# Kernel tuning notes

Measured on AMD Instinct MI355X. Metric: run time of the kernel, lower is better.

## Reference

```python
import jax, jax.numpy as jnp
import numpy as np

N_SRC, N_DST, DEG = 100000, 50000, 16
NODE_IN, EDGE_IN, HID = 128, 64, 64
E = N_DST * DEG


def sparsemax(z):
    # z: [..., K]; sparsemax along last axis (Martins & Astudillo)
    z = z - jnp.max(z, axis=-1, keepdims=True)
    zs = -jnp.sort(-z, axis=-1)  # descending sort
    k_range = jnp.arange(1, z.shape[-1] + 1, dtype=z.dtype)
    cs = jnp.cumsum(zs, axis=-1)
    is_gt = (1.0 + k_range * zs > cs).astype(z.dtype)
    k = jnp.max(is_gt * k_range, axis=-1, keepdims=True)
    tau = (jnp.sum(is_gt * zs, axis=-1, keepdims=True) - 1.0) / k
    return jnp.maximum(z - tau, 0.0)


def setup_inputs() -> dict:
    key = jax.random.key(0)
    ks = jax.random.split(key, 8)
    s = 0.02
    return {
        "node_features": jax.random.normal(ks[0], (N_SRC, NODE_IN), jnp.float32),
        "edge_features": jax.random.normal(ks[1], (E, EDGE_IN), jnp.float32),
        "src_idx": jax.random.randint(ks[2], (E,), 0, N_SRC, jnp.int32),
        "We": s * jax.random.normal(ks[3], (EDGE_IN, HID), jnp.float32),
        "be": jnp.zeros((HID,), jnp.float32),
        "Wa": s * jax.random.normal(ks[4], (EDGE_IN, HID), jnp.float32),
        "ba": jnp.zeros((HID,), jnp.float32),
        "wa": s * jax.random.normal(ks[5], (HID,), jnp.float32),
        "Wo": s * jax.random.normal(ks[6], (NODE_IN + HID, HID), jnp.float32),
        "bo": jnp.zeros((HID,), jnp.float32),
        "Wn": s * jax.random.normal(ks[7], (NODE_IN + HID, HID), jnp.float32),
        "bn": jnp.zeros((HID,), jnp.float32),
        "n_dst": N_DST,
        "deg": DEG,
    }


def reference(node_features, edge_features, src_idx, We, be, Wa, ba, wa, Wo, bo, Wn, bn, n_dst, deg):
    # dropout is identity in eval / p=0
    h_dst = node_features[:n_dst]                               # [n_dst, node_in]
    # message_func: per-edge transforms
    e_out = jax.nn.relu(edge_features @ We + be)                # [E, hid]
    a = jax.nn.leaky_relu((edge_features @ Wa + ba) @ wa)       # [E]
    h_src_e = node_features[src_idx]                            # gather [E, node_in]
    m = jax.nn.relu(jnp.concatenate([h_src_e, e_out], axis=-1) @ Wo + bo)  # [E, hid]
    # reduce_func: mailbox is [n_dst, deg, .] (fixed in-degree graph)
    a = a.reshape(n_dst, deg)
    m = m.reshape(n_dst, deg, -1)
    alpha = sparsemax(a)                                        # [n_dst, deg]
    h_neigh = jnp.einsum('nd,ndh->nh', alpha, m)                # [n_dst, hid]
    # node update
    return jax.nn.relu(jnp.concatenate([h_dst, h_neigh], axis=-1) @ Wn + bn)
```

## Files before the change

kernel.cpp:

```cpp
#include <hip/hip_runtime.h>


#define ND 50000
#define NS 100000

typedef __bf16 bf16x8 __attribute__((ext_vector_type(8)));
typedef float f32x4 __attribute__((ext_vector_type(4)));

__device__ __forceinline__ void sync_wave() {
  asm volatile("s_waitcnt lgkmcnt(0)" ::: "memory");
}

__device__ __forceinline__ unsigned short f2bf(float x) {
  unsigned u = __float_as_uint(x);
  u += 0x7fffu + ((u >> 16) & 1u);
  return (unsigned short)(u >> 16);
}
__device__ __forceinline__ float bf2f(unsigned short u) {
  return __uint_as_float((unsigned)u << 16);
}

union Frag8 { bf16x8 v; unsigned u32[4]; };

__device__ __forceinline__ bf16x8 pack8(const float* fr) {
  Frag8 f;
  #pragma unroll
  for (int j = 0; j < 4; ++j) {
    unsigned lo = __float_as_uint(fr[2 * j]) + 0x8000u;
    unsigned hi = __float_as_uint(fr[2 * j + 1]) + 0x8000u;
    f.u32[j] = __builtin_amdgcn_perm(hi, lo, 0x07060302);
  }
  return f.v;
}

#define MFMA(a, b, c) __builtin_amdgcn_mfma_f32_16x16x32_bf16((a), (b), (c), 0, 0, 0)

extern "C" __global__ void gteast_prep(const float* __restrict__ Wa,
                                       const float* __restrict__ ba,
                                       const float* __restrict__ wa,
                                       float* __restrict__ vc) {
  __shared__ float red[260];
  const int tid = threadIdx.x, k = tid >> 2, p = tid & 3;
  float s = 0.f;
  for (int h = 16 * p; h < 16 * p + 16; ++h) s += Wa[k * 64 + h] * wa[h];
  red[tid] = s;
  if (tid < 4) {
    float sc = 0.f;
    for (int h = 16 * tid; h < 16 * tid + 16; ++h) sc += ba[h] * wa[h];
    red[256 + tid] = sc;
  }
  __syncthreads();
  if (p == 0) vc[k] = red[4 * k] + red[4 * k + 1] + red[4 * k + 2] + red[4 * k + 3];
  if (tid == 0) vc[64] = red[256] + red[257] + red[258] + red[259];
}

extern "C" __global__ void __launch_bounds__(256, 3)
gteast_src(const float* __restrict__ nf, const float* __restrict__ Wo,
           unsigned short* __restrict__ y) {
  __shared__ unsigned short WuT[64 * 136];
  const int tid = threadIdx.x;
  for (int i = tid; i < 128 * 64; i += 256) {
    int k = i >> 6, n = i & 63;
    WuT[n * 136 + k] = f2bf(Wo[i]);
  }
  __syncthreads();

  const int lane = tid & 63, w = tid >> 6, q = lane >> 4, t = lane & 15;
  const int tile = blockIdx.x * 4 + w;
  if (tile >= NS / 16) return;
  const int r0 = tile * 16;

  float raw[8];
  bf16x8 af[4];
  const float* hp = nf + (long)(r0 + t) * 128 + q * 8;
  #pragma unroll
  for (int kc = 0; kc < 4; ++kc) {
    float4 a0 = *reinterpret_cast<const float4*>(hp + kc * 32);
    float4 a1 = *reinterpret_cast<const float4*>(hp + kc * 32 + 4);
    raw[0] = a0.x; raw[1] = a0.y; raw[2] = a0.z; raw[3] = a0.w;
    raw[4] = a1.x; raw[5] = a1.y; raw[6] = a1.z; raw[7] = a1.w;
    af[kc] = pack8(raw);
  }
  #pragma unroll
  for (int nt = 0; nt < 4; ++nt) {
    f32x4 c = {0.f, 0.f, 0.f, 0.f};
    #pragma unroll
    for (int kc = 0; kc < 4; ++kc)
      c = MFMA(af[kc], *reinterpret_cast<const bf16x8*>(&WuT[(nt * 16 + t) * 136 + kc * 32 + q * 8]), c);
    #pragma unroll
    for (int r = 0; r < 4; ++r)
      y[(long)(r0 + 4 * q + r) * 64 + nt * 16 + t] = f2bf(c[r]);
  }
}

extern "C" __global__ void __launch_bounds__(256, 3)
gteast_edge(const float* __restrict__ ef, const int* __restrict__ src_idx,
            const float* __restrict__ We, const float* __restrict__ be,
            const float* __restrict__ Wo, const float* __restrict__ bo,
            const float* __restrict__ vc, const unsigned short* __restrict__ y,
            float* __restrict__ hn_out) {
  __shared__ unsigned short WeT[64 * 72];
  __shared__ unsigned short WoLoT[64 * 72];
  __shared__ unsigned short Elds[4][16 * 72];
  __shared__ float vls[68];

  const int tid = threadIdx.x;
  for (int i = tid; i < 64 * 64; i += 256) {
    int k = i >> 6, n = i & 63;
    WeT[n * 72 + k] = f2bf(We[i]);
  }
  for (int i = tid; i < 64 * 64; i += 256) {
    int k = i >> 6, n = i & 63;
    WoLoT[n * 72 + k] = f2bf(Wo[(128 + k) * 64 + n]);
  }
  if (tid < 65) vls[tid] = vc[tid];
  __syncthreads();

  const int lane = tid & 63, w = tid >> 6;
  const int q = lane >> 4, t = lane & 15;
  const int wid = blockIdx.x * 4 + w;
  if (wid * 8 >= ND) return;

  unsigned short* E = Elds[w];
  const float cval = vls[64];
  float beL[4], boL[4];
  #pragma unroll
  for (int nt = 0; nt < 4; ++nt) { beL[nt] = be[nt * 16 + t]; boL[nt] = bo[nt * 16 + t]; }
  float vsl[16];
  #pragma unroll
  for (int j = 0; j < 8; ++j) { vsl[j] = vls[q * 8 + j]; vsl[8 + j] = vls[32 + q * 8 + j]; }

  const int si0 = src_idx[wid * 128 + lane];
  const int si1 = src_idx[wid * 128 + 64 + lane];

  const long ebase = (long)(wid * 128);

  float4 efn[4];
  {
    const float* er = ef + (ebase + t) * 64 + q * 8;
    efn[0] = *reinterpret_cast<const float4*>(er);
    efn[1] = *reinterpret_cast<const float4*>(er + 4);
    efn[2] = *reinterpret_cast<const float4*>(er + 32);
    efn[3] = *reinterpret_cast<const float4*>(er + 36);
  }
  unsigned short yv[16];
  #pragma unroll
  for (int r = 0; r < 4; ++r) {
    const int s0 = __shfl(si0, 4 * q + r);
    const unsigned short* yp = y + (long)s0 * 64 + t;
    #pragma unroll
    for (int nt = 0; nt < 4; ++nt) yv[r * 4 + nt] = yp[nt * 16];
  }

  for (int it = 0; it < 8; ++it) {
    const int n = wid * 8 + it;
    const int itn = it < 7 ? it + 1 : 7;

    float fe[16];
    fe[0] = efn[0].x; fe[1] = efn[0].y; fe[2] = efn[0].z; fe[3] = efn[0].w;
    fe[4] = efn[1].x; fe[5] = efn[1].y; fe[6] = efn[1].z; fe[7] = efn[1].w;
    fe[8] = efn[2].x; fe[9] = efn[2].y; fe[10] = efn[2].z; fe[11] = efn[2].w;
    fe[12] = efn[3].x; fe[13] = efn[3].y; fe[14] = efn[3].z; fe[15] = efn[3].w;
    {
      const float* er = ef + (ebase + itn * 16 + t) * 64 + q * 8;
      efn[0] = *reinterpret_cast<const float4*>(er);
      efn[1] = *reinterpret_cast<const float4*>(er + 4);
      efn[2] = *reinterpret_cast<const float4*>(er + 32);
      efn[3] = *reinterpret_cast<const float4*>(er + 36);
    }

    float ap = 0.f;
    #pragma unroll
    for (int j = 0; j < 16; ++j) ap += fe[j] * vsl[j];
    ap += __shfl_xor(ap, 16);
    ap += __shfl_xor(ap, 32);
    float a = ap + cval;
    a = a > 0.f ? a : 0.01f * a;

    const bf16x8 e0 = pack8(fe), e1 = pack8(fe + 8);
    #pragma unroll
    for (int nt = 0; nt < 4; ++nt) {
      f32x4 c = {0.f, 0.f, 0.f, 0.f};
      c = MFMA(e0, *reinterpret_cast<const bf16x8*>(&WeT[(nt * 16 + t) * 72 + q * 8]), c);
      c = MFMA(e1, *reinterpret_cast<const bf16x8*>(&WeT[(nt * 16 + t) * 72 + 32 + q * 8]), c);
      #pragma unroll
      for (int r = 0; r < 4; ++r) {
        float vv = fmaxf(c[r] + beL[nt], 0.f);
        E[(4 * q + r) * 72 + nt * 16 + t] = f2bf(vv);
      }
    }
    sync_wave();

    bf16x8 af4 = *reinterpret_cast<const bf16x8*>(&E[t * 72 + q * 8]);
    bf16x8 af5 = *reinterpret_cast<const bf16x8*>(&E[t * 72 + 32 + q * 8]);

    f32x4 accM[4];
    #pragma unroll
    for (int nt = 0; nt < 4; ++nt) {
      f32x4 c = {0.f, 0.f, 0.f, 0.f};
      c = MFMA(af4, *reinterpret_cast<const bf16x8*>(&WoLoT[(nt * 16 + t) * 72 + q * 8]), c);
      c = MFMA(af5, *reinterpret_cast<const bf16x8*>(&WoLoT[(nt * 16 + t) * 72 + 32 + q * 8]), c);
      #pragma unroll
      for (int r = 0; r < 4; ++r)
        c[r] = fmaxf(c[r] + bf2f(yv[r * 4 + nt]) + boL[nt], 0.f);
      accM[nt] = c;
    }
    sync_wave();

    #pragma unroll
    for (int r = 0; r < 4; ++r) {
      const int idx = 16 * itn + 4 * q + r;
      const int sn = (itn < 4) ? __shfl(si0, idx) : __shfl(si1, idx - 64);
      const unsigned short* yp = y + (long)sn * 64 + t;
      #pragma unroll
      for (int nt = 0; nt < 4; ++nt) yv[r * 4 + nt] = yp[nt * 16];
    }

    const float z = a;
    float cp = 0.f, sp = 0.f;
    #pragma unroll
    for (int r = 0; r < 4; ++r) {
      float zj = __shfl(z, 4 * q + r, 16);
      const bool ge = (zj >= z);
      cp += ge ? 1.f : 0.f;
      sp += ge ? zj : 0.f;
    }
    cp += __shfl_xor(cp, 16); sp += __shfl_xor(sp, 16);
    cp += __shfl_xor(cp, 32); sp += __shfl_xor(sp, 32);
    const bool valid = 1.f + cp * z > sp;
    float kf = valid ? cp : 0.f;
    float sv = valid ? sp : 0.f;
    #pragma unroll
    for (int m = 1; m < 16; m <<= 1) {
      float ok = __shfl_xor(kf, m), os = __shfl_xor(sv, m);
      if (ok > kf) { kf = ok; sv = os; }
    }
    const float tau = (sv - 1.f) / kf;
    const float alpha = fmaxf(a - tau, 0.f);

    float al[4];
    #pragma unroll
    for (int r = 0; r < 4; ++r) al[r] = __shfl(alpha, 4 * q + r);
    float p[4];
    #pragma unroll
    for (int nt = 0; nt < 4; ++nt) {
      p[nt] = al[0] * accM[nt][0] + al[1] * accM[nt][1] +
              al[2] * accM[nt][2] + al[3] * accM[nt][3];
      p[nt] += __shfl_xor(p[nt], 16);
      p[nt] += __shfl_xor(p[nt], 32);
    }
    const float pown = (q == 0) ? p[0] : (q == 1) ? p[1] : (q == 2) ? p[2] : p[3];
    hn_out[(long)n * 64 + lane] = pown;
  }
}

extern "C" __global__ void __launch_bounds__(256, 3)
gteast_edge_fb(const float* __restrict__ nf, const float* __restrict__ ef,
               const int* __restrict__ src_idx,
               const float* __restrict__ We, const float* __restrict__ be,
               const float* __restrict__ Wo, const float* __restrict__ bo,
               const float* __restrict__ vc,
               float* __restrict__ hn_out) {
  __shared__ unsigned short WeT[64 * 72];
  __shared__ unsigned short WoT[64 * 200];
  __shared__ unsigned short Elds[4][16 * 72];
  __shared__ float vls[68];

  const int tid = threadIdx.x;
  for (int i = tid; i < 64 * 64; i += 256) {
    int k = i >> 6, n = i & 63;
    WeT[n * 72 + k] = f2bf(We[i]);
  }
  for (int i = tid; i < 192 * 64; i += 256) {
    int k = i >> 6, n = i & 63;
    WoT[n * 200 + k] = f2bf(Wo[i]);
  }
  if (tid < 65) vls[tid] = vc[tid];
  __syncthreads();

  const int lane = tid & 63, w = tid >> 6;
  const int q = lane >> 4, t = lane & 15;
  const int wid = blockIdx.x * 4 + w;
  if (wid * 8 >= ND) return;

  unsigned short* E = Elds[w];
  const float cval = vls[64];
  float beL[4], boL[4];
  #pragma unroll
  for (int nt = 0; nt < 4; ++nt) { beL[nt] = be[nt * 16 + t]; boL[nt] = bo[nt * 16 + t]; }
  float vsl[16];
  #pragma unroll
  for (int j = 0; j < 8; ++j) { vsl[j] = vls[q * 8 + j]; vsl[8 + j] = vls[32 + q * 8 + j]; }

  const int si0 = src_idx[wid * 128 + lane];
  const int si1 = src_idx[wid * 128 + 64 + lane];
  const long ebase = (long)(wid * 128);

  float4 efn[4];
  {
    const float* er = ef + (ebase + t) * 64 + q * 8;
    efn[0] = *reinterpret_cast<const float4*>(er);
    efn[1] = *reinterpret_cast<const float4*>(er + 4);
    efn[2] = *reinterpret_cast<const float4*>(er + 32);
    efn[3] = *reinterpret_cast<const float4*>(er + 36);
  }
  float hraw[32];
  {
    const int s0 = __shfl(si0, t);
    const float* hp = nf + (long)s0 * 128 + q * 8;
    #pragma unroll
    for (int kc = 0; kc < 4; ++kc) {
      float4 a0 = *reinterpret_cast<const float4*>(hp + kc * 32);
      float4 a1 = *reinterpret_cast<const float4*>(hp + kc * 32 + 4);
      hraw[kc * 8 + 0] = a0.x; hraw[kc * 8 + 1] = a0.y; hraw[kc * 8 + 2] = a0.z; hraw[kc * 8 + 3] = a0.w;
      hraw[kc * 8 + 4] = a1.x; hraw[kc * 8 + 5] = a1.y; hraw[kc * 8 + 6] = a1.z; hraw[kc * 8 + 7] = a1.w;
    }
  }

  for (int it = 0; it < 8; ++it) {
    const int n = wid * 8 + it;
    const int itn = it < 7 ? it + 1 : 7;

    float fe[16];
    fe[0] = efn[0].x; fe[1] = efn[0].y; fe[2] = efn[0].z; fe[3] = efn[0].w;
    fe[4] = efn[1].x; fe[5] = efn[1].y; fe[6] = efn[1].z; fe[7] = efn[1].w;
    fe[8] = efn[2].x; fe[9] = efn[2].y; fe[10] = efn[2].z; fe[11] = efn[2].w;
    fe[12] = efn[3].x; fe[13] = efn[3].y; fe[14] = efn[3].z; fe[15] = efn[3].w;
    {
      const float* er = ef + (ebase + itn * 16 + t) * 64 + q * 8;
      efn[0] = *reinterpret_cast<const float4*>(er);
      efn[1] = *reinterpret_cast<const float4*>(er + 4);
      efn[2] = *reinterpret_cast<const float4*>(er + 32);
      efn[3] = *reinterpret_cast<const float4*>(er + 36);
    }

    float ap = 0.f;
    #pragma unroll
    for (int j = 0; j < 16; ++j) ap += fe[j] * vsl[j];
    ap += __shfl_xor(ap, 16);
    ap += __shfl_xor(ap, 32);
    float a = ap + cval;
    a = a > 0.f ? a : 0.01f * a;

    const bf16x8 e0 = pack8(fe), e1 = pack8(fe + 8);
    #pragma unroll
    for (int nt = 0; nt < 4; ++nt) {
      f32x4 c = {0.f, 0.f, 0.f, 0.f};
      c = MFMA(e0, *reinterpret_cast<const bf16x8*>(&WeT[(nt * 16 + t) * 72 + q * 8]), c);
      c = MFMA(e1, *reinterpret_cast<const bf16x8*>(&WeT[(nt * 16 + t) * 72 + 32 + q * 8]), c);
      #pragma unroll
      for (int r = 0; r < 4; ++r) {
        float vv = fmaxf(c[r] + beL[nt], 0.f);
        E[(4 * q + r) * 72 + nt * 16 + t] = f2bf(vv);
      }
    }
    sync_wave();

    bf16x8 af[6];
    #pragma unroll
    for (int kc = 0; kc < 4; ++kc) af[kc] = pack8(hraw + kc * 8);
    af[4] = *reinterpret_cast<const bf16x8*>(&E[t * 72 + q * 8]);
    af[5] = *reinterpret_cast<const bf16x8*>(&E[t * 72 + 32 + q * 8]);

    {
      const int sn = (itn < 4) ? __shfl(si0, 16 * itn + t)
                               : __shfl(si1, 16 * (itn - 4) + t);
      const float* hp = nf + (long)sn * 128 + q * 8;
      #pragma unroll
      for (int kc = 0; kc < 4; ++kc) {
        float4 a0 = *reinterpret_cast<const float4*>(hp + kc * 32);
        float4 a1 = *reinterpret_cast<const float4*>(hp + kc * 32 + 4);
        hraw[kc * 8 + 0] = a0.x; hraw[kc * 8 + 1] = a0.y; hraw[kc * 8 + 2] = a0.z; hraw[kc * 8 + 3] = a0.w;
        hraw[kc * 8 + 4] = a1.x; hraw[kc * 8 + 5] = a1.y; hraw[kc * 8 + 6] = a1.z; hraw[kc * 8 + 7] = a1.w;
      }
    }

    f32x4 accM[4];
    #pragma unroll
    for (int nt = 0; nt < 4; ++nt) {
      f32x4 c = {0.f, 0.f, 0.f, 0.f};
      #pragma unroll
      for (int kc = 0; kc < 6; ++kc)
        c = MFMA(af[kc], *reinterpret_cast<const bf16x8*>(&WoT[(nt * 16 + t) * 200 + kc * 32 + q * 8]), c);
      #pragma unroll
      for (int r = 0; r < 4; ++r) c[r] = fmaxf(c[r] + boL[nt], 0.f);
      accM[nt] = c;
    }
    sync_wave();

    float zz = a;
    #pragma unroll
    for (int k = 2; k <= 16; k <<= 1) {
      #pragma unroll
      for (int j = k >> 1; j > 0; j >>= 1) {
        float o = __shfl_xor(zz, j);
        const bool upper = (t & j) != 0;
        const bool desc = (t & k) == 0;
        zz = (upper != desc) ? fmaxf(zz, o) : fminf(zz, o);
      }
    }
    float cs = zz;
    #pragma unroll
    for (int off = 1; off < 16; off <<= 1) {
      float o = __shfl_up(cs, off, 16);
      cs += (t >= off) ? o : 0.f;
    }
    const bool gt = 1.f + (float)(t + 1) * zz > cs;
    float kf = gt ? (float)(t + 1) : 0.f;
    float sv = gt ? zz : 0.f;
    #pragma unroll
    for (int m = 1; m < 16; m <<= 1) {
      kf = fmaxf(kf, __shfl_xor(kf, m));
      sv += __shfl_xor(sv, m);
    }
    const float tau = (sv - 1.f) / kf;
    const float alpha = fmaxf(a - tau, 0.f);

    float al[4];
    #pragma unroll
    for (int r = 0; r < 4; ++r) al[r] = __shfl(alpha, 4 * q + r);
    float p[4];
    #pragma unroll
    for (int nt = 0; nt < 4; ++nt) {
      p[nt] = al[0] * accM[nt][0] + al[1] * accM[nt][1] +
              al[2] * accM[nt][2] + al[3] * accM[nt][3];
      p[nt] += __shfl_xor(p[nt], 16);
      p[nt] += __shfl_xor(p[nt], 32);
    }
    const float pown = (q == 0) ? p[0] : (q == 1) ? p[1] : (q == 2) ? p[2] : p[3];
    hn_out[(long)n * 64 + lane] = pown;
  }
}

extern "C" __global__ void __launch_bounds__(256, 3)
gteast_out(const float* __restrict__ nf, const float* __restrict__ Wn,
           const float* __restrict__ bn, float* __restrict__ out) {
  __shared__ unsigned short WnT[64 * 200];
  const int tid = threadIdx.x;
  for (int i = tid; i < 192 * 64; i += 256) {
    int k = i >> 6, nn = i & 63;
    WnT[nn * 200 + k] = f2bf(Wn[i]);
  }
  __syncthreads();

  const int lane = tid & 63, w = tid >> 6, q = lane >> 4, t = lane & 15;
  const int tile = blockIdx.x * 4 + w;
  if (tile >= ND / 16) return;
  const int r0 = tile * 16;

  float bnL[4];
  #pragma unroll
  for (int nt = 0; nt < 4; ++nt) bnL[nt] = bn[nt * 16 + t];

  float raw[8];
  bf16x8 af[6];
  const float* hp = nf + (long)(r0 + t) * 128 + q * 8;
  #pragma unroll
  for (int kc = 0; kc < 4; ++kc) {
    float4 a0 = *reinterpret_cast<const float4*>(hp + kc * 32);
    float4 a1 = *reinterpret_cast<const float4*>(hp + kc * 32 + 4);
    raw[0] = a0.x; raw[1] = a0.y; raw[2] = a0.z; raw[3] = a0.w;
    raw[4] = a1.x; raw[5] = a1.y; raw[6] = a1.z; raw[7] = a1.w;
    af[kc] = pack8(raw);
  }
  const float* gp = out + (long)(r0 + t) * 64 + q * 8;
  #pragma unroll
  for (int kc = 0; kc < 2; ++kc) {
    float4 a0 = *reinterpret_cast<const float4*>(gp + kc * 32);
    float4 a1 = *reinterpret_cast<const float4*>(gp + kc * 32 + 4);
    raw[0] = a0.x; raw[1] = a0.y; raw[2] = a0.z; raw[3] = a0.w;
    raw[4] = a1.x; raw[5] = a1.y; raw[6] = a1.z; raw[7] = a1.w;
    af[4 + kc] = pack8(raw);
  }

  #pragma unroll
  for (int nt = 0; nt < 4; ++nt) {
    f32x4 c = {0.f, 0.f, 0.f, 0.f};
    #pragma unroll
    for (int kc = 0; kc < 6; ++kc)
      c = MFMA(af[kc], *reinterpret_cast<const bf16x8*>(&WnT[(nt * 16 + t) * 200 + kc * 32 + q * 8]), c);
    #pragma unroll
    for (int r = 0; r < 4; ++r)
      out[(long)(r0 + 4 * q + r) * 64 + nt * 16 + t] = fmaxf(c[r] + bnL[nt], 0.f);
  }
}

extern "C" void kernel_launch(void* const* d_in, const int* in_sizes, int n_in,
                              void* d_out, int out_size, void* d_ws, size_t ws_size,
                              hipStream_t stream) {
  const float* nf = (const float*)d_in[0];
  const float* ef = (const float*)d_in[1];
  const int* si   = (const int*)d_in[2];
  const float* We = (const float*)d_in[3];
  const float* be = (const float*)d_in[4];
  const float* Wa = (const float*)d_in[5];
  const float* ba = (const float*)d_in[6];
  const float* wa = (const float*)d_in[7];
  const float* Wo = (const float*)d_in[8];
  const float* bo = (const float*)d_in[9];
  const float* Wn = (const float*)d_in[10];
  const float* bn = (const float*)d_in[11];
  float* out = (float*)d_out;
  float* vc = (float*)d_ws;

  const size_t yneed = 512 + (size_t)NS * 64 * sizeof(unsigned short);

  gteast_prep<<<1, 256, 0, stream>>>(Wa, ba, wa, vc);
  if (ws_size >= yneed) {
    unsigned short* y = (unsigned short*)((char*)d_ws + 512);
    gteast_src<<<1563, 256, 0, stream>>>(nf, Wo, y);
    gteast_edge<<<1563, 256, 0, stream>>>(ef, si, We, be, Wo, bo, vc, y, out);
  } else {
    gteast_edge_fb<<<1563, 256, 0, stream>>>(nf, ef, si, We, be, Wo, bo, vc, out);
  }
  gteast_out<<<782, 256, 0, stream>>>(nf, Wn, bn, out);
}
```

Baseline: 373.5 us.

## Precompute node-update source term in src kernel and vectorize y gathers

```diff
diff --git a/kernel.cpp b/kernel.cpp
--- a/kernel.cpp
+++ b/kernel.cpp
@@ -6,6 +6,7 @@
 
 typedef __bf16 bf16x8 __attribute__((ext_vector_type(8)));
 typedef float f32x4 __attribute__((ext_vector_type(4)));
+typedef unsigned short u16x4 __attribute__((ext_vector_type(4)));
 
 __device__ __forceinline__ void sync_wave() {
   asm volatile("s_waitcnt lgkmcnt(0)" ::: "memory");
@@ -56,12 +57,15 @@
 
 extern "C" __global__ void __launch_bounds__(256, 3)
 gteast_src(const float* __restrict__ nf, const float* __restrict__ Wo,
-           unsigned short* __restrict__ y) {
+           const float* __restrict__ Wn,
+           unsigned short* __restrict__ y, unsigned short* __restrict__ z) {
   __shared__ unsigned short WuT[64 * 136];
+  __shared__ unsigned short WnuT[64 * 136];
   const int tid = threadIdx.x;
   for (int i = tid; i < 128 * 64; i += 256) {
     int k = i >> 6, n = i & 63;
     WuT[n * 136 + k] = f2bf(Wo[i]);
+    WnuT[n * 136 + k] = f2bf(Wn[i]);
   }
   __syncthreads();
 
@@ -81,15 +85,37 @@
     raw[4] = a1.x; raw[5] = a1.y; raw[6] = a1.z; raw[7] = a1.w;
     af[kc] = pack8(raw);
   }
+
+  f32x4 accY[4];
   #pragma unroll
   for (int nt = 0; nt < 4; ++nt) {
     f32x4 c = {0.f, 0.f, 0.f, 0.f};
     #pragma unroll
     for (int kc = 0; kc < 4; ++kc)
       c = MFMA(af[kc], *reinterpret_cast<const bf16x8*>(&WuT[(nt * 16 + t) * 136 + kc * 32 + q * 8]), c);
-    #pragma unroll
-    for (int r = 0; r < 4; ++r)
-      y[(long)(r0 + 4 * q + r) * 64 + nt * 16 + t] = f2bf(c[r]);
+    accY[nt] = c;
+  }
+  #pragma unroll
+  for (int r = 0; r < 4; ++r) {
+    u16x4 v = {f2bf(accY[0][r]), f2bf(accY[1][r]), f2bf(accY[2][r]), f2bf(accY[3][r])};
+    *reinterpret_cast<u16x4*>(y + (long)(r0 + 4 * q + r) * 64 + t * 4) = v;
+  }
+
+  if (tile < ND / 16) {
+    f32x4 accZ[4];
+    #pragma unroll
+    for (int nt = 0; nt < 4; ++nt) {
+      f32x4 c = {0.f, 0.f, 0.f, 0.f};
+      #pragma unroll
+      for (int kc = 0; kc < 4; ++kc)
+        c = MFMA(af[kc], *reinterpret_cast<const bf16x8*>(&WnuT[(nt * 16 + t) * 136 + kc * 32 + q * 8]), c);
+      accZ[nt] = c;
+    }
+    #pragma unroll
+    for (int r = 0; r < 4; ++r) {
+      u16x4 v = {f2bf(accZ[0][r]), f2bf(accZ[1][r]), f2bf(accZ[2][r]), f2bf(accZ[3][r])};
+      *reinterpret_cast<u16x4*>(z + (long)(r0 + 4 * q + r) * 64 + t * 4) = v;
+    }
   }
 }
 
@@ -143,13 +169,11 @@
     efn[2] = *reinterpret_cast<const float4*>(er + 32);
     efn[3] = *reinterpret_cast<const float4*>(er + 36);
   }
-  unsigned short yv[16];
+  u16x4 yv[4];
   #pragma unroll
   for (int r = 0; r < 4; ++r) {
     const int s0 = __shfl(si0, 4 * q + r);
-    const unsigned short* yp = y + (long)s0 * 64 + t;
-    #pragma unroll
-    for (int nt = 0; nt < 4; ++nt) yv[r * 4 + nt] = yp[nt * 16];
+    yv[r] = *reinterpret_cast<const u16x4*>(y + (long)s0 * 64 + t * 4);
   }
 
   for (int it = 0; it < 8; ++it) {
@@ -202,7 +226,7 @@
       c = MFMA(af5, *reinterpret_cast<const bf16x8*>(&WoLoT[(nt * 16 + t) * 72 + 32 + q * 8]), c);
       #pragma unroll
       for (int r = 0; r < 4; ++r)
-        c[r] = fmaxf(c[r] + bf2f(yv[r * 4 + nt]) + boL[nt], 0.f);
+        c[r] = fmaxf(c[r] + bf2f(yv[r][nt]) + boL[nt], 0.f);
       accM[nt] = c;
     }
     sync_wave();
@@ -210,10 +234,8 @@
     #pragma unroll
     for (int r = 0; r < 4; ++r) {
       const int idx = 16 * itn + 4 * q + r;
-      const int sn = (itn < 4) ? __shfl(si0, idx) : __shfl(si1, idx - 64);
-      const unsigned short* yp = y + (long)sn * 64 + t;
-      #pragma unroll
-      for (int nt = 0; nt < 4; ++nt) yv[r * 4 + nt] = yp[nt * 16];
+      const int sn = (idx < 64) ? __shfl(si0, idx) : __shfl(si1, idx - 64);
+      yv[r] = *reinterpret_cast<const u16x4*>(y + (long)sn * 64 + t * 4);
     }
 
     const float z = a;
@@ -251,6 +273,58 @@
     }
     const float pown = (q == 0) ? p[0] : (q == 1) ? p[1] : (q == 2) ? p[2] : p[3];
     hn_out[(long)n * 64 + lane] = pown;
+  }
+}
+
+extern "C" __global__ void __launch_bounds__(256, 4)
+gteast_out(const unsigned short* __restrict__ z, const float* __restrict__ Wn,
+           const float* __restrict__ bn, float* __restrict__ out) {
+  __shared__ unsigned short WnLoT[64 * 72];
+  const int tid = threadIdx.x;
+  for (int i = tid; i < 64 * 64; i += 256) {
+    int k = i >> 6, nn = i & 63;
+    WnLoT[nn * 72 + k] = f2bf(Wn[(128 + k) * 64 + nn]);
+  }
+  __syncthreads();
+
+  const int lane = tid & 63, w = tid >> 6, q = lane >> 4, t = lane & 15;
+  const int tile = blockIdx.x * 4 + w;
+  if (tile >= ND / 16) return;
+  const int r0 = tile * 16;
+
+  float bnL[4];
+  #pragma unroll
+  for (int nt = 0; nt < 4; ++nt) bnL[nt] = bn[nt * 16 + t];
+
+  float raw[8];
+  bf16x8 af4, af5;
+  const float* gp = out + (long)(r0 + t) * 64 + q * 8;
+  {
+    float4 a0 = *reinterpret_cast<const float4*>(gp);
+    float4 a1 = *reinterpret_cast<const float4*>(gp + 4);
+    raw[0] = a0.x; raw[1] = a0.y; raw[2] = a0.z; raw[3] = a0.w;
+    raw[4] = a1.x; raw[5] = a1.y; raw[6] = a1.z; raw[7] = a1.w;
+    af4 = pack8(raw);
+    a0 = *reinterpret_cast<const float4*>(gp + 32);
+    a1 = *reinterpret_cast<const float4*>(gp + 36);
+    raw[0] = a0.x; raw[1] = a0.y; raw[2] = a0.z; raw[3] = a0.w;
+    raw[4] = a1.x; raw[5] = a1.y; raw[6] = a1.z; raw[7] = a1.w;
+    af5 = pack8(raw);
+  }
+  u16x4 zv[4];
+  #pragma unroll
+  for (int r = 0; r < 4; ++r)
+    zv[r] = *reinterpret_cast<const u16x4*>(z + (long)(r0 + 4 * q + r) * 64 + t * 4);
+
+  #pragma unroll
+  for (int nt = 0; nt < 4; ++nt) {
+    f32x4 c = {0.f, 0.f, 0.f, 0.f};
+    c = MFMA(af4, *reinterpret_cast<const bf16x8*>(&WnLoT[(nt * 16 + t) * 72 + q * 8]), c);
+    c = MFMA(af5, *reinterpret_cast<const bf16x8*>(&WnLoT[(nt * 16 + t) * 72 + 32 + q * 8]), c);
+    #pragma unroll
+    for (int r = 0; r < 4; ++r)
+      out[(long)(r0 + 4 * q + r) * 64 + nt * 16 + t] =
+          fmaxf(c[r] + bf2f(zv[r][nt]) + bnL[nt], 0.f);
   }
 }
 
@@ -433,8 +507,8 @@
 }
 
 extern "C" __global__ void __launch_bounds__(256, 3)
-gteast_out(const float* __restrict__ nf, const float* __restrict__ Wn,
-           const float* __restrict__ bn, float* __restrict__ out) {
+gteast_out_fb(const float* __restrict__ nf, const float* __restrict__ Wn,
+              const float* __restrict__ bn, float* __restrict__ out) {
   __shared__ unsigned short WnT[64 * 200];
   const int tid = threadIdx.x;
   for (int i = tid; i < 192 * 64; i += 256) {
@@ -503,15 +577,17 @@
   float* out = (float*)d_out;
   float* vc = (float*)d_ws;
 
-  const size_t yneed = 512 + (size_t)NS * 64 * sizeof(unsigned short);
+  const size_t yneed = 512 + (size_t)NS * 64 * 2 + (size_t)ND * 64 * 2;
 
   gteast_prep<<<1, 256, 0, stream>>>(Wa, ba, wa, vc);
   if (ws_size >= yneed) {
     unsigned short* y = (unsigned short*)((char*)d_ws + 512);
-    gteast_src<<<1563, 256, 0, stream>>>(nf, Wo, y);
+    unsigned short* z = y + (size_t)NS * 64;
+    gteast_src<<<1563, 256, 0, stream>>>(nf, Wo, Wn, y, z);
     gteast_edge<<<1563, 256, 0, stream>>>(ef, si, We, be, Wo, bo, vc, y, out);
+    gteast_out<<<782, 256, 0, stream>>>(z, Wn, bn, out);
   } else {
     gteast_edge_fb<<<1563, 256, 0, stream>>>(nf, ef, si, We, be, Wo, bo, vc, out);
-  }
-  gteast_out<<<782, 256, 0, stream>>>(nf, Wn, bn, out);
-}
+    gteast_out_fb<<<782, 256, 0, stream>>>(nf, Wn, bn, out);
+  }
+}
```

Result: no change. 370.0 us (-0.9%).
